# Performance work log

Hardware: AMD Instinct MI355X
Metric: run time of the kernel (lower is better)

Reference implementation:

```python
import jax, jax.numpy as jnp
import numpy as np

SIGMA = 3.0
NUM_CLASSES = 10


def _nearest_resize(x, out_h, out_w):
    # torch F.interpolate default 'nearest': src_idx = floor(dst_idx * in/out)
    in_h, in_w = x.shape[-2], x.shape[-1]
    rows = (jnp.arange(out_h) * in_h) // out_h
    cols = (jnp.arange(out_w) * in_w) // out_w
    return x[..., rows, :][..., :, cols]


def _forward(feats, centers, idx, labels, img_h, img_w):
    # Gaussian heatmap per user input at image resolution: [B,N,H,W]
    xs = jnp.arange(img_w, dtype=jnp.float32) + 0.5  # pixel-centre xs
    ys = jnp.arange(img_h, dtype=jnp.float32) + 0.5
    alpha = -0.5 / (SIGMA ** 2)
    cx = centers[..., 0][..., None, None]  # [B,N,1,1]
    cy = centers[..., 1][..., None, None]
    heat = jnp.exp(alpha * ((xs[None, None, None, :] - cx) ** 2
                            + (ys[None, None, :, None] - cy) ** 2))
    valid = (idx != -1)[..., None, None]  # idx == -1 rows stay zero
    heat = jnp.where(valid, heat, jnp.zeros((), heat.dtype))

    cls_ids = jnp.arange(1, NUM_CLASSES + 1)
    cmask = labels[:, None, :] == cls_ids[None, :, None]  # [B,K,N]
    any_cls = jnp.any(cmask, axis=-1)                     # [B,K]

    outs = []
    for feat in feats:
        H, W = feat.shape[-2], feat.shape[-1]
        h = _nearest_resize(heat, H, W)                               # [B,N,H,W]
        h = h / (jnp.sum(h, axis=(-2, -1), keepdims=True) + 1e-8)
        # template (eq 1): spatially weighted average feature vector
        tmpl = jnp.einsum('bchw,bnhw->bnc', feat, h)                  # [B,N,C]
        # correlation (eq 2): 1x1 conv of feat with per-sample template
        cor = jnp.einsum('bnc,bchw->bnhw', tmpl, feat)                # [B,N,H,W]
        # class-wise collate: max over user inputs whose label == class
        neg = jnp.finfo(cor.dtype).min
        masked = jnp.where(cmask[..., None, None], cor[:, None], neg)  # [B,K,N,H,W]
        cmax = jnp.max(masked, axis=2)                                 # [B,K,H,W]
        cmax = jnp.where(any_cls[..., None, None], cmax, jnp.zeros((), cmax.dtype))
        outs.append(jnp.concatenate([feat, cmax], axis=1))             # [B,C+K,H,W]
    return tuple(outs)


def setup_inputs() -> dict:
    key = jax.random.key(0)
    k0, k1, k2, kc, ki, kl = jax.random.split(key, 6)
    B, C, N = 2, 256, 64
    img_h, img_w = 512, 512
    x0 = jax.random.normal(k0, (B, C, 64, 64), dtype=jnp.float32)
    x1 = jax.random.normal(k1, (B, C, 32, 32), dtype=jnp.float32)
    x2 = jax.random.normal(k2, (B, C, 16, 16), dtype=jnp.float32)
    centers = jax.random.uniform(kc, (B, N, 2), dtype=jnp.float32) * jnp.array([img_w, img_h], dtype=jnp.float32)
    idx = jnp.where(jax.random.uniform(ki, (B, N)) < 0.1, -1, 0).astype(jnp.int64)
    labels = jax.random.randint(kl, (B, N), 1, NUM_CLASSES + 1).astype(jnp.int64)
    return {"x0": x0, "x1": x1, "x2": x2, "centers": centers,
            "idx": idx, "labels": labels, "img_h": img_h, "img_w": img_w}


def reference(x0, x1, x2, centers, idx, labels, img_h, img_w):
    return _forward((x0, x1, x2), centers, idx, labels, img_h, img_w)
```

## Files before the change

### kernel.cpp

```cpp
#include <hip/hip_runtime.h>
#include <hip/hip_bf16.h>
#include <cfloat>
#include <cmath>

namespace {
constexpr int NB = 2;
constexpr int NN = 64;
constexpr int NC = 256;
constexpr int NK = 10;
constexpr float ALPHA = -1.0f / 18.0f;
constexpr int TMPL_FLOATS = 3 * NB * NC * NN;
constexpr int PART_FLOATS = 42 * 4 * NK * 256;
}

__device__ __forceinline__ bool sniff_f32(const void* x0) {
  const ushort4 v = ((const ushort4*)x0)[threadIdx.x & 63];
  bool bad = (((v.x >> 7) & 0xFF) >= 137) | (((v.y >> 7) & 0xFF) >= 137) |
             (((v.z >> 7) & 0xFF) >= 137) | (((v.w >> 7) & 0xFF) >= 137);
  return __ballot(bad) != 0ULL;
}

__device__ __forceinline__ float ldf(const void* p, size_t i, bool f32) {
  return f32 ? ((const float*)p)[i]
             : __bfloat162float(((const __hip_bfloat16*)p)[i]);
}
__device__ __forceinline__ float bf2f(unsigned short u) {
  return __uint_as_float((unsigned)u << 16);
}

__device__ __forceinline__ void tile_decode(int tile, int& lvl, int& b, int& tl) {
  if (tile < 32)      { lvl = 0; b = tile >> 4; tl = tile & 15; }
  else if (tile < 40) { const int t = tile - 32; lvl = 1; b = t >> 2; tl = t & 3; }
  else                { lvl = 2; b = tile - 40; tl = 0; }
}

__global__ __launch_bounds__(256) void tmpl_kernel(
    const void* __restrict__ x0, const void* __restrict__ x1,
    const void* __restrict__ x2, const void* __restrict__ centers,
    const int* __restrict__ idxp, const int* __restrict__ labels,
    float* __restrict__ tmpl_t) {
  const bool f32 = sniff_f32(x0);
  const int bx  = blockIdx.x;
  const int lvl = bx >> 7;
  const int b   = (bx >> 6) & 1;
  const int n   = bx & 63;
  const int W   = 64 >> lvl;
  const int HW  = W * W;
  const float s = (float)(8 << lvl);
  const void* feat = (lvl == 0) ? x0 : (lvl == 1) ? x1 : x2;

  __shared__ float ex[64], ey[64];
  __shared__ float sh_inv;
  __shared__ int   sh_win[4];

  const int t = threadIdx.x;
  const float cx = ldf(centers, (size_t)(b * NN + n) * 2 + 0, f32);
  const float cy = ldf(centers, (size_t)(b * NN + n) * 2 + 1, f32);

  if (t < W) {
    const float dx = (float)t * s + 0.5f - cx;
    const float dy = (float)t * s + 0.5f - cy;
    ex[t] = expf(ALPHA * dx * dx);
    ey[t] = expf(ALPHA * dy * dy);
  }
  __syncthreads();

  if (t == 0) {
    const bool i64 = (labels[1] == 0);
    const int  m   = b * NN + n;
    const int  iv  = i64 ? idxp[2 * m] : idxp[m];
    float Sx = 0.f, Sy = 0.f;
    for (int i = 0; i < W; ++i) { Sx += ex[i]; Sy += ey[i]; }
    sh_inv = (iv != -1) ? 1.0f / (Sx * Sy + 1e-8f) : 0.0f;
    int cs = (int)floorf((cx - 0.5f) / s + 0.5f); cs = min(max(cs, 0), W - 1);
    int rs = (int)floorf((cy - 0.5f) / s + 0.5f); rs = min(max(rs, 0), W - 1);
    const float tx = ex[cs] * 1e-7f, ty = ey[rs] * 1e-7f;
    int clo = cs, chi = cs, rlo = rs, rhi = rs;
    while (clo > 0     && ex[clo - 1] >= tx) --clo;
    while (chi < W - 1 && ex[chi + 1] >= tx) ++chi;
    while (rlo > 0     && ey[rlo - 1] >= ty) --rlo;
    while (rhi < W - 1 && ey[rhi + 1] >= ty) ++rhi;
    sh_win[0] = clo; sh_win[1] = chi; sh_win[2] = rlo; sh_win[3] = rhi;
  }
  __syncthreads();

  const float inv = sh_inv;
  const int clo = sh_win[0], chi = sh_win[1], rlo = sh_win[2], rhi = sh_win[3];
  const size_t cbase = (size_t)(b * NC + t) * HW;
  float acc = 0.f;
  for (int r = rlo; r <= rhi; ++r) {
    float rowa = 0.f;
    for (int c = clo; c <= chi; ++c)
      rowa += ex[c] * ldf(feat, cbase + r * W + c, f32);
    acc += ey[r] * rowa;
  }
  tmpl_t[(((size_t)lvl * NB + b) * NC + t) * NN + n] = acc * inv;
}

__global__ __launch_bounds__(256, 1) void cor_kernel(
    const void* __restrict__ x0, const void* __restrict__ x1,
    const void* __restrict__ x2, const int* __restrict__ labels,
    const float* __restrict__ tmpl_t, float* __restrict__ part,
    float* __restrict__ out) {
  const bool f32 = sniff_f32(x0);
  const int bx   = blockIdx.x;
  const int tile = bx >> 2, q = bx & 3;
  int lvl, b, tl;
  tile_decode(tile, lvl, b, tl);
  const int W = 64 >> lvl, HW = W * W;
  const int lane = threadIdx.x & 63;
  const int wv   = __builtin_amdgcn_readfirstlane(threadIdx.x >> 6);
  const int px   = tl * 256 + lane * 4;
  const void* feat = (lvl == 0) ? x0 : (lvl == 1) ? x1 : x2;
  const size_t base1 = (size_t)NB * (NC + NK) * 4096;
  const size_t base2 = base1 + (size_t)NB * (NC + NK) * 1024;
  const size_t lvl_base = (lvl == 0) ? 0 : (lvl == 1) ? base1 : base2;
  float* ob = out + lvl_base + (size_t)b * (NC + NK) * HW + px;

  __shared__ float tlds[NC][16];
  __shared__ float kmb[4][NK][64][4];
  __shared__ int   lab[16];

  {
    const float4* s4 =
        (const float4*)(tmpl_t + (size_t)(lvl * NB + b) * NC * NN);
    float4* d4 = (float4*)&tlds[0][0];
#pragma unroll
    for (int k = 0; k < 4; ++k) {
      const int m = threadIdx.x + k * 256;
      d4[m] = s4[(size_t)(m >> 2) * 16 + q * 4 + (m & 3)];
    }
  }
  if (threadIdx.x < 16) {
    const bool i64 = (labels[1] == 0);
    const int  m   = b * NN + q * 16 + threadIdx.x;
    lab[threadIdx.x] = i64 ? labels[2 * m] : labels[m];
  }
  __syncthreads();

  float4 acc[4];
#pragma unroll
  for (int j = 0; j < 4; ++j) acc[j] = float4{0.f, 0.f, 0.f, 0.f};

  auto run = [&](auto loadf) {
    float4 fpre[4];
#pragma unroll
    for (int k = 0; k < 4; ++k) fpre[k] = loadf(k);
#pragma unroll 4
    for (int c = 0; c < NC; ++c) {
      const float4 f = fpre[c & 3];
      fpre[c & 3] = loadf(min(c + 4, NC - 1));
      if (q == 0 && wv == (c >> 6))
        *(float4*)&ob[(size_t)c * HW] = f;
      const float4 tv = *(const float4*)&tlds[c][wv * 4];
      acc[0].x += tv.x * f.x; acc[0].y += tv.x * f.y;
      acc[0].z += tv.x * f.z; acc[0].w += tv.x * f.w;
      acc[1].x += tv.y * f.x; acc[1].y += tv.y * f.y;
      acc[1].z += tv.y * f.z; acc[1].w += tv.y * f.w;
      acc[2].x += tv.z * f.x; acc[2].y += tv.z * f.y;
      acc[2].z += tv.z * f.z; acc[2].w += tv.z * f.w;
      acc[3].x += tv.w * f.x; acc[3].y += tv.w * f.y;
      acc[3].z += tv.w * f.z; acc[3].w += tv.w * f.w;
    }
  };
  if (f32) {
    const float* fp = (const float*)feat + (size_t)b * NC * HW + px;
    run([&](int c) { return *(const float4*)&fp[(size_t)c * HW]; });
  } else {
    const unsigned short* hp =
        (const unsigned short*)feat + (size_t)b * NC * HW + px;
    run([&](int c) {
      const ushort4 v = *(const ushort4*)&hp[(size_t)c * HW];
      return float4{bf2f(v.x), bf2f(v.y), bf2f(v.z), bf2f(v.w)};
    });
  }

  float4 km[NK];
#pragma unroll
  for (int k = 0; k < NK; ++k) km[k] = float4{-FLT_MAX, -FLT_MAX, -FLT_MAX, -FLT_MAX};
#pragma unroll
  for (int j = 0; j < 4; ++j) {
    const int L = lab[wv * 4 + j];
#pragma unroll
    for (int kk = 1; kk <= NK; ++kk)
      if (L == kk) {
        km[kk - 1].x = fmaxf(km[kk - 1].x, acc[j].x);
        km[kk - 1].y = fmaxf(km[kk - 1].y, acc[j].y);
        km[kk - 1].z = fmaxf(km[kk - 1].z, acc[j].z);
        km[kk - 1].w = fmaxf(km[kk - 1].w, acc[j].w);
      }
  }
#pragma unroll
  for (int k = 0; k < NK; ++k) *(float4*)&kmb[wv][k][lane][0] = km[k];
  __syncthreads();

  if (wv == 0) {
    float* pp = part + ((size_t)(tile * 4 + q) * NK) * 256 + lane * 4;
#pragma unroll
    for (int k = 0; k < NK; ++k) {
      float4 m = *(float4*)&kmb[0][k][lane][0];
#pragma unroll
      for (int w = 1; w < 4; ++w) {
        const float4 o = *(float4*)&kmb[w][k][lane][0];
        m.x = fmaxf(m.x, o.x); m.y = fmaxf(m.y, o.y);
        m.z = fmaxf(m.z, o.z); m.w = fmaxf(m.w, o.w);
      }
      *(float4*)&pp[(size_t)k * 256] = m;
    }
  }
}

__global__ __launch_bounds__(256) void combine_kernel(
    const float* __restrict__ part, float* __restrict__ out) {
  const int tile = blockIdx.x;
  int lvl, b, tl;
  tile_decode(tile, lvl, b, tl);
  const int W = 64 >> lvl, HW = W * W;
  const int px = tl * 256 + threadIdx.x;
  const size_t base1 = (size_t)NB * (NC + NK) * 4096;
  const size_t base2 = base1 + (size_t)NB * (NC + NK) * 1024;
  const size_t lvl_base = (lvl == 0) ? 0 : (lvl == 1) ? base1 : base2;
  float* ob = out + lvl_base + (size_t)b * (NC + NK) * HW + px;
  const float* pp = part + (size_t)tile * 4 * NK * 256 + threadIdx.x;

#pragma unroll
  for (int k = 0; k < NK; ++k) {
    float m = -FLT_MAX;
#pragma unroll
    for (int q = 0; q < 4; ++q)
      m = fmaxf(m, pp[(size_t)(q * NK + k) * 256]);
    ob[(size_t)(NC + k) * HW] = (m == -FLT_MAX) ? 0.f : m;
  }
}

extern "C" void kernel_launch(void* const* d_in, const int* in_sizes, int n_in,
                              void* d_out, int out_size, void* d_ws, size_t ws_size,
                              hipStream_t stream) {
  const void* x0 = d_in[0];
  const void* x1 = d_in[1];
  const void* x2 = d_in[2];
  const void* ce = d_in[3];
  const int* idxp   = (const int*)d_in[4];
  const int* labels = (const int*)d_in[5];
  float* tmpl = (float*)d_ws;
  float* part = tmpl + TMPL_FLOATS;
  float* out  = (float*)d_out;

  tmpl_kernel<<<3 * NB * NN, 256, 0, stream>>>(x0, x1, x2, ce, idxp, labels, tmpl);
  cor_kernel<<<168, 256, 0, stream>>>(x0, x1, x2, labels, tmpl, part, out);
  combine_kernel<<<42, 256, 0, stream>>>(part, out);
}
```

Before: 116.9 us.

## Split cor_kernel channel reduction across four wave groups per block

```diff
diff --git a/kernel.cpp b/kernel.cpp
--- a/kernel.cpp
+++ b/kernel.cpp
@@ -97,7 +97,7 @@
   tmpl_t[(((size_t)lvl * NB + b) * NC + t) * NN + n] = acc * inv;
 }
 
-__global__ __launch_bounds__(256, 1) void cor_kernel(
+__global__ __launch_bounds__(1024, 1) void cor_kernel(
     const void* __restrict__ x0, const void* __restrict__ x1,
     const void* __restrict__ x2, const int* __restrict__ labels,
     const float* __restrict__ tmpl_t, float* __restrict__ part,
@@ -110,6 +110,8 @@
   const int W = 64 >> lvl, HW = W * W;
   const int lane = threadIdx.x & 63;
   const int wv   = __builtin_amdgcn_readfirstlane(threadIdx.x >> 6);
+  const int nsub = wv & 3;
+  const int cq   = wv >> 2;
   const int px   = tl * 256 + lane * 4;
   const void* feat = (lvl == 0) ? x0 : (lvl == 1) ? x1 : x2;
   const size_t base1 = (size_t)NB * (NC + NK) * 4096;
@@ -118,6 +120,7 @@
   float* ob = out + lvl_base + (size_t)b * (NC + NK) * HW + px;
 
   __shared__ float tlds[NC][16];
+  __shared__ float pl[4][16][64][4];
   __shared__ float kmb[4][NK][64][4];
   __shared__ int   lab[16];
 
@@ -125,11 +128,8 @@
     const float4* s4 =
         (const float4*)(tmpl_t + (size_t)(lvl * NB + b) * NC * NN);
     float4* d4 = (float4*)&tlds[0][0];
-#pragma unroll
-    for (int k = 0; k < 4; ++k) {
-      const int m = threadIdx.x + k * 256;
-      d4[m] = s4[(size_t)(m >> 2) * 16 + q * 4 + (m & 3)];
-    }
+    const int m = threadIdx.x;
+    d4[m] = s4[(size_t)(m >> 2) * 16 + q * 4 + (m & 3)];
   }
   if (threadIdx.x < 16) {
     const bool i64 = (labels[1] == 0);
@@ -142,17 +142,19 @@
 #pragma unroll
   for (int j = 0; j < 4; ++j) acc[j] = float4{0.f, 0.f, 0.f, 0.f};
 
+  const int c0 = cq * 64;
   auto run = [&](auto loadf) {
     float4 fpre[4];
 #pragma unroll
-    for (int k = 0; k < 4; ++k) fpre[k] = loadf(k);
+    for (int k = 0; k < 4; ++k) fpre[k] = loadf(c0 + k);
 #pragma unroll 4
-    for (int c = 0; c < NC; ++c) {
-      const float4 f = fpre[c & 3];
-      fpre[c & 3] = loadf(min(c + 4, NC - 1));
-      if (q == 0 && wv == (c >> 6))
+    for (int i = 0; i < 64; ++i) {
+      const int c = c0 + i;
+      const float4 f = fpre[i & 3];
+      fpre[i & 3] = loadf(min(c + 4, NC - 1));
+      if (q == 0 && nsub == 0)
         *(float4*)&ob[(size_t)c * HW] = f;
-      const float4 tv = *(const float4*)&tlds[c][wv * 4];
+      const float4 tv = *(const float4*)&tlds[c][nsub * 4];
       acc[0].x += tv.x * f.x; acc[0].y += tv.x * f.y;
       acc[0].z += tv.x * f.z; acc[0].w += tv.x * f.w;
       acc[1].x += tv.y * f.x; acc[1].y += tv.y * f.y;
@@ -175,23 +177,40 @@
     });
   }
 
-  float4 km[NK];
-#pragma unroll
-  for (int k = 0; k < NK; ++k) km[k] = float4{-FLT_MAX, -FLT_MAX, -FLT_MAX, -FLT_MAX};
-#pragma unroll
-  for (int j = 0; j < 4; ++j) {
-    const int L = lab[wv * 4 + j];
-#pragma unroll
-    for (int kk = 1; kk <= NK; ++kk)
-      if (L == kk) {
-        km[kk - 1].x = fmaxf(km[kk - 1].x, acc[j].x);
-        km[kk - 1].y = fmaxf(km[kk - 1].y, acc[j].y);
-        km[kk - 1].z = fmaxf(km[kk - 1].z, acc[j].z);
-        km[kk - 1].w = fmaxf(km[kk - 1].w, acc[j].w);
-      }
-  }
-#pragma unroll
-  for (int k = 0; k < NK; ++k) *(float4*)&kmb[wv][k][lane][0] = km[k];
+#pragma unroll
+  for (int j = 0; j < 4; ++j)
+    *(float4*)&pl[cq][nsub * 4 + j][lane][0] = acc[j];
+  __syncthreads();
+
+  if (cq == 0) {
+    float4 km[NK];
+#pragma unroll
+    for (int k = 0; k < NK; ++k)
+      km[k] = float4{-FLT_MAX, -FLT_MAX, -FLT_MAX, -FLT_MAX};
+#pragma unroll
+    for (int j = 0; j < 4; ++j) {
+      const int n16 = nsub * 4 + j;
+      const float4 p0 = *(float4*)&pl[0][n16][lane][0];
+      const float4 p1 = *(float4*)&pl[1][n16][lane][0];
+      const float4 p2 = *(float4*)&pl[2][n16][lane][0];
+      const float4 p3 = *(float4*)&pl[3][n16][lane][0];
+      const float4 tot = float4{p0.x + p1.x + p2.x + p3.x,
+                                p0.y + p1.y + p2.y + p3.y,
+                                p0.z + p1.z + p2.z + p3.z,
+                                p0.w + p1.w + p2.w + p3.w};
+      const int L = lab[n16];
+#pragma unroll
+      for (int kk = 1; kk <= NK; ++kk)
+        if (L == kk) {
+          km[kk - 1].x = fmaxf(km[kk - 1].x, tot.x);
+          km[kk - 1].y = fmaxf(km[kk - 1].y, tot.y);
+          km[kk - 1].z = fmaxf(km[kk - 1].z, tot.z);
+          km[kk - 1].w = fmaxf(km[kk - 1].w, tot.w);
+        }
+    }
+#pragma unroll
+    for (int k = 0; k < NK; ++k) *(float4*)&kmb[nsub][k][lane][0] = km[k];
+  }
   __syncthreads();
 
   if (wv == 0) {
@@ -247,6 +266,6 @@
   float* out  = (float*)d_out;
 
   tmpl_kernel<<<3 * NB * NN, 256, 0, stream>>>(x0, x1, x2, ce, idxp, labels, tmpl);
-  cor_kernel<<<168, 256, 0, stream>>>(x0, x1, x2, labels, tmpl, part, out);
+  cor_kernel<<<168, 1024, 0, stream>>>(x0, x1, x2, labels, tmpl, part, out);
   combine_kernel<<<42, 256, 0, stream>>>(part, out);
 }
```

Result: faster. 101.6 us (-13.0%).
